# Kernel tuning notes

Hardware: AMD Instinct MI355X
Metric: run time of the kernel (lower is better)

## Reference

```python
import jax, jax.numpy as jnp
import numpy as np

N_DRUG = 572
EMB = 512
K_NB = 64
SEG_NB = 16
BN_EPS = 1e-5


def setup_inputs() -> dict:
    key = jax.random.key(0)
    ks = jax.random.split(key, 8)
    return {
        "drug_name": jnp.arange(N_DRUG, dtype=jnp.int64) if jax.config.jax_enable_x64 else jnp.arange(N_DRUG, dtype=jnp.int32),
        "adj_tail": jax.random.randint(ks[0], (N_DRUG, K_NB), 0, 100000),
        "adj_relation": jax.random.randint(ks[1], (N_DRUG, K_NB), 0, 200),
        "inv_adj_idx": jax.random.randint(ks[2], (N_DRUG, SEG_NB), 0, N_DRUG),
        "drug_table": jax.random.normal(ks[3], (N_DRUG, EMB), dtype=jnp.float32),
        "rela_table": jax.random.normal(ks[4], (200, EMB), dtype=jnp.float32),
        "ent_table": jax.random.normal(ks[5], (100000, EMB), dtype=jnp.float32),
        "W_lin": jax.random.normal(ks[6], (2 * EMB, EMB), dtype=jnp.float32) * (1.0 / np.sqrt(2 * EMB)),
        "b_lin": jnp.zeros((EMB,), jnp.float32),
        "bn_gamma": jnp.ones((EMB,), jnp.float32),
        "bn_beta": jnp.zeros((EMB,), jnp.float32),
        "epoch": 2,
    }


def _forward(drug_name, adj_tail, adj_relation, inv_adj_idx,
             drug_table, rela_table, ent_table, W_lin, b_lin,
             bn_gamma, bn_beta, epoch):
    # Embedding gathers
    drug_emb = drug_table[drug_name]          # [N, D]
    rel_emb = rela_table[adj_relation]        # [N, K, D]
    ent_emb = ent_table[adj_tail]             # [N, K, D]

    # KGCN-style attention over sampled neighbors: score_k = softmax(drug . rel_k)
    scores = jax.nn.softmax(jnp.einsum('nd,nkd->nk', drug_emb, rel_emb), axis=1)
    attended = jnp.einsum('nk,nkd->nd', scores, ent_emb)  # [N, D]

    # Linear -> ReLU -> BatchNorm1d (training-mode batch stats, biased var)
    e = jnp.concatenate([attended, drug_emb], axis=1)     # [N, 2D]
    h = jax.nn.relu(e @ W_lin + b_lin)                    # [N, D]
    mu = jnp.mean(h, axis=0)
    var = jnp.mean(jnp.square(h - mu), axis=0)
    drug_f = bn_gamma * (h - mu) * jax.lax.rsqrt(var + BN_EPS) + bn_beta

    if epoch > 1:
        # Sequential in-place neighbor averaging (faithful to the Python loop:
        # later drugs see already-updated rows).
        def body(f, x):
            i, pos = x
            avg = jnp.mean(f[pos], axis=0)                # [D]
            f = f.at[i].set((avg + f[i]) * 0.5)
            return f, None
        idxs = jnp.arange(N_DRUG)
        drug_f, _ = jax.lax.scan(body, drug_f, (idxs, inv_adj_idx))
    return drug_f


def reference(drug_name, adj_tail, adj_relation, inv_adj_idx,
              drug_table, rela_table, ent_table, W_lin, b_lin,
              bn_gamma, bn_beta, epoch):
    return _forward(drug_name, adj_tail, adj_relation, inv_adj_idx,
                    drug_table, rela_table, ent_table, W_lin, b_lin,
                    bn_gamma, bn_beta, epoch)
```

## Files before the change

kernel.cpp:

```cpp
#include <hip/hip_runtime.h>
#include <hip/hip_bf16.h>

#define N_DRUG 572
#define EMB    512
#define K_NB   64
#define SEG_NB 16
#define SCOLS  16
#define DPB    4

typedef __hip_bfloat16  bf16;
typedef __hip_bfloat162 bf162;

__device__ __forceinline__ float b2f(bf16 x){ return __bfloat162float(x); }

template<typename T> __device__ __forceinline__ float ldf(const T* p);
template<> __device__ __forceinline__ float ldf<float>(const float* p){ return *p; }
template<> __device__ __forceinline__ float ldf<bf16>(const bf16* p){ return b2f(*p); }

template<typename T> __device__ __forceinline__ float2 ld2(const T* p);
template<> __device__ __forceinline__ float2 ld2<float>(const float* p){ return *(const float2*)p; }
template<> __device__ __forceinline__ float2 ld2<bf16>(const bf16* p){
    bf162 v = *(const bf162*)p; return make_float2(b2f(v.x), b2f(v.y));
}

template<typename T> __device__ __forceinline__ void st2(T* p, float x, float y);
template<> __device__ __forceinline__ void st2<float>(float* p, float x, float y){ *(float2*)p = make_float2(x, y); }
template<> __device__ __forceinline__ void st2<bf16>(bf16* p, float x, float y){
    bf162 v; v.x = __float2bfloat16(x); v.y = __float2bfloat16(y); *(bf162*)p = v;
}

__device__ __forceinline__ bool idx_is64(const void* drug_name) {
    return ((const int*)drug_name)[1] == 0;
}
__device__ __forceinline__ int ld_idx(const void* p, int i, bool is64) {
    return is64 ? (int)((const long long*)p)[i] : ((const int*)p)[i];
}

__device__ __forceinline__ bool detect_bf16(const void* tab) {
    const int lane = threadIdx.x & 63;
    int hit = 0;
    if (lane < 32) {
        const unsigned u = ((const unsigned*)tab)[lane * 997];
        const unsigned e = (u >> 7) & 0xffu;
        hit = (e >= 110u && e <= 141u) ? 1 : 0;
    }
    return __popcll(__ballot(hit)) >= 24;
}

struct __align__(16) FwdSmem {
    float e[DPB][2 * EMB];
    float sc[DPB][K_NB];
    int   tl[DPB][K_NB];
    int   rl[DPB][K_NB];
};

template<typename T>
__device__ void fwd_impl(FwdSmem& sm,
    const void* drug_name, const void* adj_tail, const void* adj_rel,
    const T* __restrict__ drug_table, const T* __restrict__ rela_table,
    const T* __restrict__ ent_table,  const T* __restrict__ W,
    const T* __restrict__ bl, T* __restrict__ h)
{
    const int  t    = threadIdx.x;
    const int  n0   = blockIdx.x * DPB;
    const bool is64 = idx_is64(drug_name);

    #pragma unroll
    for (int dr = 0; dr < DPB; ++dr) {
        const int row = ld_idx(drug_name, n0 + dr, is64);
        const float2 v = ld2(drug_table + (size_t)row * EMB + 2 * t);
        sm.e[dr][EMB + 2 * t]     = v.x;
        sm.e[dr][EMB + 2 * t + 1] = v.y;
    }
    {
        const int dr = t >> 6, k = t & 63;
        sm.tl[dr][k] = ld_idx(adj_tail, n0 * K_NB + t, is64);
        sm.rl[dr][k] = ld_idx(adj_rel,  n0 * K_NB + t, is64);
    }
    __syncthreads();

    {
        const int wave = t >> 6, lane = t & 63;
        const int g = lane >> 4, c = lane & 15;
        const float* ed = &sm.e[wave][EMB];
        #pragma unroll 2
        for (int pass = 0; pass < 16; ++pass) {
            const int k = pass * 4 + g;
            const T* rl = rela_table + (size_t)sm.rl[wave][k] * EMB;
            float p = 0.f;
            #pragma unroll
            for (int m = 0; m < 16; ++m) {
                const int dd = 2 * c + 32 * m;
                const float2 rv = ld2(rl + dd);
                const float2 ev = *(const float2*)&ed[dd];
                p = fmaf(ev.x, rv.x, p);
                p = fmaf(ev.y, rv.y, p);
            }
            p += __shfl_xor(p, 1, 64);
            p += __shfl_xor(p, 2, 64);
            p += __shfl_xor(p, 4, 64);
            p += __shfl_xor(p, 8, 64);
            if (c == 0) sm.sc[wave][k] = p;
        }
    }
    __syncthreads();

    {
        const int dr = t >> 6, k = t & 63;
        const float s = sm.sc[dr][k];
        float m = s;
        #pragma unroll
        for (int off = 32; off; off >>= 1) m = fmaxf(m, __shfl_xor(m, off, 64));
        const float ex = __expf(s - m);
        float sum = ex;
        #pragma unroll
        for (int off = 32; off; off >>= 1) sum += __shfl_xor(sum, off, 64);
        sm.sc[dr][k] = ex / sum;
    }
    __syncthreads();

    {
        float a0[DPB], a1[DPB];
        #pragma unroll
        for (int dr = 0; dr < DPB; ++dr) { a0[dr] = 0.f; a1[dr] = 0.f; }
        #pragma unroll 2
        for (int k = 0; k < K_NB; ++k) {
            #pragma unroll
            for (int dr = 0; dr < DPB; ++dr) {
                const float w  = sm.sc[dr][k];
                const float2 v = ld2(ent_table + (size_t)sm.tl[dr][k] * EMB + 2 * t);
                a0[dr] = fmaf(w, v.x, a0[dr]);
                a1[dr] = fmaf(w, v.y, a1[dr]);
            }
        }
        #pragma unroll
        for (int dr = 0; dr < DPB; ++dr) {
            sm.e[dr][2 * t]     = a0[dr];
            sm.e[dr][2 * t + 1] = a1[dr];
        }
    }
    __syncthreads();

    {
        const int d0 = 2 * t;
        const float2 bb = ld2(bl + d0);
        float a0[DPB], a1[DPB];
        #pragma unroll
        for (int dr = 0; dr < DPB; ++dr) { a0[dr] = bb.x; a1[dr] = bb.y; }
        #pragma unroll 2
        for (int q = 0; q < (2 * EMB) / 4; ++q) {
            const T* Wp = W + (size_t)(4 * q) * EMB + d0;
            const float2 w0 = ld2(Wp);
            const float2 w1 = ld2(Wp + EMB);
            const float2 w2 = ld2(Wp + 2 * EMB);
            const float2 w3 = ld2(Wp + 3 * EMB);
            #pragma unroll
            for (int dr = 0; dr < DPB; ++dr) {
                const float4 f = ((const float4*)&sm.e[dr][0])[q];
                a0[dr] = fmaf(f.x, w0.x, a0[dr]); a1[dr] = fmaf(f.x, w0.y, a1[dr]);
                a0[dr] = fmaf(f.y, w1.x, a0[dr]); a1[dr] = fmaf(f.y, w1.y, a1[dr]);
                a0[dr] = fmaf(f.z, w2.x, a0[dr]); a1[dr] = fmaf(f.z, w2.y, a1[dr]);
                a0[dr] = fmaf(f.w, w3.x, a0[dr]); a1[dr] = fmaf(f.w, w3.y, a1[dr]);
            }
        }
        #pragma unroll
        for (int dr = 0; dr < DPB; ++dr)
            st2(h + (size_t)(n0 + dr) * EMB + d0,
                fmaxf(a0[dr], 0.f), fmaxf(a1[dr], 0.f));
    }
}

__global__ __launch_bounds__(256) void k_fwd(
    const void* drug_name, const void* adj_tail, const void* adj_rel,
    const void* drug_tab, const void* rela_tab, const void* ent_tab,
    const void* W, const void* bl, void* h)
{
    __shared__ FwdSmem sm;
    if (detect_bf16(drug_tab))
        fwd_impl<bf16>(sm, drug_name, adj_tail, adj_rel,
                       (const bf16*)drug_tab, (const bf16*)rela_tab,
                       (const bf16*)ent_tab, (const bf16*)W,
                       (const bf16*)bl, (bf16*)h);
    else
        fwd_impl<float>(sm, drug_name, adj_tail, adj_rel,
                        (const float*)drug_tab, (const float*)rela_tab,
                        (const float*)ent_tab, (const float*)W,
                        (const float*)bl, (float*)h);
}

struct __align__(16) ScanSmem {
    float    fbuf[N_DRUG * SCOLS];
    unsigned obuf[N_DRUG * SEG_NB];
    float4   corr[576];
};

__device__ __forceinline__ float bflo(unsigned u){ return __uint_as_float(u << 16); }
__device__ __forceinline__ float bfhi(unsigned u){ return __uint_as_float(u & 0xffff0000u); }
__device__ __forceinline__ unsigned pack_bf2(float a, float b) {
    bf162 v; v.x = __float2bfloat16(a); v.y = __float2bfloat16(b);
    unsigned u; __builtin_memcpy(&u, &v, 4); return u;
}

template<typename T>
__device__ __forceinline__ void stage_fbuf(float* fbuf, const T* h, int c0, int t);
template<>
__device__ __forceinline__ void stage_fbuf<float>(float* fbuf, const float* h, int c0, int t) {
    float4* dst = (float4*)fbuf;
    #pragma unroll 4
    for (int k = t; k < N_DRUG * 4; k += 64)
        dst[k] = *(const float4*)(h + (size_t)(k >> 2) * EMB + c0 + 4 * (k & 3));
}
template<>
__device__ __forceinline__ void stage_fbuf<bf16>(float* fbuf, const bf16* h, int c0, int t) {
    float4* dst = (float4*)fbuf;
    #pragma unroll 4
    for (int k = t; k < N_DRUG * 2; k += 64) {
        const uint4 v = *(const uint4*)(h + (size_t)(k >> 1) * EMB + c0 + 8 * (k & 1));
        dst[2 * k]     = make_float4(bflo(v.x), bfhi(v.x), bflo(v.y), bfhi(v.y));
        dst[2 * k + 1] = make_float4(bflo(v.z), bfhi(v.z), bflo(v.w), bfhi(v.w));
    }
}

template<typename T>
__device__ __forceinline__ void flush_fbuf(const float* fbuf, T* h, int c0, int t);
template<>
__device__ __forceinline__ void flush_fbuf<float>(const float* fbuf, float* h, int c0, int t) {
    const float4* src = (const float4*)fbuf;
    #pragma unroll 4
    for (int k = t; k < N_DRUG * 4; k += 64)
        *(float4*)(h + (size_t)(k >> 2) * EMB + c0 + 4 * (k & 3)) = src[k];
}
template<>
__device__ __forceinline__ void flush_fbuf<bf16>(const float* fbuf, bf16* h, int c0, int t) {
    const float4* src = (const float4*)fbuf;
    #pragma unroll 4
    for (int k = t; k < N_DRUG * 2; k += 64) {
        const float4 f0 = src[2 * k], f1 = src[2 * k + 1];
        uint4 o;
        o.x = pack_bf2(f0.x, f0.y); o.y = pack_bf2(f0.z, f0.w);
        o.z = pack_bf2(f1.x, f1.y); o.w = pack_bf2(f1.z, f1.w);
        *(uint4*)(h + (size_t)(k >> 1) * EMB + c0 + 8 * (k & 1)) = o;
    }
}

template<bool IS64>
__device__ __forceinline__ void stage_obuf(unsigned* obuf, const void* inv, int t) {
    const uint4* src = (const uint4*)inv;
    if (IS64) {
        #pragma unroll 4
        for (int k = t; k < (N_DRUG * SEG_NB) / 2; k += 64) {
            const uint4 v = src[k];
            *(uint2*)(obuf + 2 * k) = make_uint2(v.x << 4, v.z << 4);
        }
    } else {
        uint4* dst = (uint4*)obuf;
        #pragma unroll 4
        for (int k = t; k < (N_DRUG * SEG_NB) / 4; k += 64) {
            uint4 v = src[k];
            v.x <<= 4; v.y <<= 4; v.z <<= 4; v.w <<= 4;
            dst[k] = v;
        }
    }
}

#define RMIN(X) (((X) < N_DRUG) ? (X) : (N_DRUG - 1))

#define BODY4(Vg, Qg, Sc, Fc, Cc, Vr, Sr, I)                                 \
    {                                                                        \
        Vg.x = fb[Qg.x + c]; Vg.y = fb[Qg.y + c];                            \
        Vg.z = fb[Qg.z + c]; Vg.w = fb[Qg.w + c];                            \
        Qg = ob4[RMIN((I) + 7) * 4 + g];                                     \
        float nv = fmaf(Sc, 1.f / 32.f, Fc * 0.5f);                          \
        nv = fmaf(Cc.x, nv1 - f1, nv);                                       \
        nv = fmaf(Cc.y, nv2 - f2, nv);                                       \
        nv = fmaf(Cc.z, nv3 - f3, nv);                                       \
        f3 = f2; f2 = f1; f1 = Fc; nv3 = nv2; nv2 = nv1; nv1 = nv;           \
        if (g == 0) sm.fbuf[(I) * SCOLS + c] = nv;                           \
        Fc = fb[RMIN((I) + 4) * 16 + c];                                     \
        Cc = sm.corr[(I) + 4];                                               \
        float l = (Vr.x + Vr.y) + (Vr.z + Vr.w);                             \
        Sr = (l + __shfl_xor(l, 16, 64)) +                                   \
             (__shfl_xor(l, 32, 64) + __shfl_xor(l, 48, 64));                \
    }

template<typename T, bool IS64>
__device__ void scan_impl(ScanSmem& sm, T* __restrict__ h,
    const void* __restrict__ inv, const T* __restrict__ gamma,
    const T* __restrict__ beta, const void* __restrict__ epoch)
{
    const int t  = threadIdx.x;
    const int c0 = blockIdx.x * SCOLS;

    stage_obuf<IS64>(sm.obuf, inv, t);
    stage_fbuf<T>(sm.fbuf, h, c0, t);
    for (int k = t; k < 576; k += 64) sm.corr[k] = make_float4(0.f, 0.f, 0.f, 0.f);
    __syncthreads();

    for (int i = 1 + t; i < N_DRUG; i += 64) {
        const unsigned tA = (unsigned)(i - 1) << 4;
        const unsigned tB = (unsigned)(i - 2) << 4;
        const unsigned tC = (unsigned)(i - 3) << 4;
        int cA = 0, cB = 0, cC = 0;
        #pragma unroll
        for (int j = 0; j < SEG_NB; ++j) {
            const unsigned o = sm.obuf[i * SEG_NB + j];
            cA += (o == tA) ? 1 : 0;
            cB += (o == tB) ? 1 : 0;
            cC += (o == tC) ? 1 : 0;
        }
        sm.corr[i] = make_float4((float)cA * (1.f / 32.f),
                                 (float)cB * (1.f / 32.f),
                                 (float)cC * (1.f / 32.f), 0.f);
    }

    {
        const int c = t & 15, g = t >> 4;
        float s = 0.f, s2 = 0.f;
        for (int r = g; r < N_DRUG; r += 4) {
            const float x = sm.fbuf[r * SCOLS + c];
            s += x; s2 = fmaf(x, x, s2);
        }
        s  += __shfl_xor(s, 16, 64);  s  += __shfl_xor(s, 32, 64);
        s2 += __shfl_xor(s2, 16, 64); s2 += __shfl_xor(s2, 32, 64);
        const float mu  = s * (1.f / N_DRUG);
        const float var = fmaxf(s2 * (1.f / N_DRUG) - mu * mu, 0.f);
        const float gs  = ldf(gamma + c0 + c) * rsqrtf(var + 1e-5f);
        const float bs  = ldf(beta  + c0 + c);
        for (int r = g; r < N_DRUG; r += 4) {
            const float x = sm.fbuf[r * SCOLS + c];
            sm.fbuf[r * SCOLS + c] = fmaf(x - mu, gs, bs);
        }
    }
    __syncthreads();

    if (((const int*)epoch)[0] > 1) {
        const int c = t & 15, g = t >> 4;
        const float* fb  = sm.fbuf;
        const uint4* ob4 = (const uint4*)sm.obuf;

        float4 V0, V1, V2, V3;
        uint4  Q0, Q1, Q2, Q3;

        {
            const uint4 o0 = ob4[0 * 4 + g], o1 = ob4[1 * 4 + g], o2 = ob4[2 * 4 + g];
            V0.x = fb[o0.x + c]; V0.y = fb[o0.y + c];
            V0.z = fb[o0.z + c]; V0.w = fb[o0.w + c];
            V1.x = fb[o1.x + c]; V1.y = fb[o1.y + c];
            V1.z = fb[o1.z + c]; V1.w = fb[o1.w + c];
            V2.x = fb[o2.x + c]; V2.y = fb[o2.y + c];
            V2.z = fb[o2.z + c]; V2.w = fb[o2.w + c];
        }
        Q3 = ob4[3 * 4 + g];
        Q0 = ob4[4 * 4 + g]; Q1 = ob4[5 * 4 + g]; Q2 = ob4[6 * 4 + g];
        float F0 = fb[0 * 16 + c], F1 = fb[1 * 16 + c];
        float F2 = fb[2 * 16 + c], F3 = fb[3 * 16 + c];
        float4 C0 = sm.corr[0], C1 = sm.corr[1];
        float4 C2 = sm.corr[2], C3 = sm.corr[3];
        float S0, S1, S2 = 0.f, S3 = 0.f;
        {
            float l0 = (V0.x + V0.y) + (V0.z + V0.w);
            S0 = (l0 + __shfl_xor(l0, 16, 64)) +
                 (__shfl_xor(l0, 32, 64) + __shfl_xor(l0, 48, 64));
            float l1 = (V1.x + V1.y) + (V1.z + V1.w);
            S1 = (l1 + __shfl_xor(l1, 16, 64)) +
                 (__shfl_xor(l1, 32, 64) + __shfl_xor(l1, 48, 64));
        }
        float nv1 = 0.f, nv2 = 0.f, nv3 = 0.f, f1 = 0.f, f2 = 0.f, f3 = 0.f;

        for (int i = 0; i < N_DRUG; i += 4) {
            BODY4(V3, Q3, S0, F0, C0, V2, S2, i);
            BODY4(V0, Q0, S1, F1, C1, V3, S3, i + 1);
            BODY4(V1, Q1, S2, F2, C2, V0, S0, i + 2);
            BODY4(V2, Q2, S3, F3, C3, V1, S1, i + 3);
        }
    }
    __syncthreads();

    flush_fbuf<T>(sm.fbuf, h, c0, t);
}

__global__ __launch_bounds__(64) void k_scan(
    void* h, const void* inv, const void* gamma, const void* beta,
    const void* epoch, const void* drug_name, const void* drug_tab)
{
    __shared__ ScanSmem sm;
    const bool isbf = detect_bf16(drug_tab);
    const bool is64 = idx_is64(drug_name);
    if (isbf) {
        if (is64) scan_impl<bf16, true >(sm, (bf16*)h, inv, (const bf16*)gamma, (const bf16*)beta, epoch);
        else      scan_impl<bf16, false>(sm, (bf16*)h, inv, (const bf16*)gamma, (const bf16*)beta, epoch);
    } else {
        if (is64) scan_impl<float, true >(sm, (float*)h, inv, (const float*)gamma, (const float*)beta, epoch);
        else      scan_impl<float, false>(sm, (float*)h, inv, (const float*)gamma, (const float*)beta, epoch);
    }
}

extern "C" void kernel_launch(void* const* d_in, const int* in_sizes, int n_in,
                              void* d_out, int out_size, void* d_ws, size_t ws_size,
                              hipStream_t stream)
{
    (void)in_sizes; (void)n_in; (void)out_size; (void)d_ws; (void)ws_size;

    k_fwd<<<N_DRUG / DPB, 256, 0, stream>>>(
        d_in[0], d_in[1], d_in[2],
        d_in[4], d_in[5], d_in[6],
        d_in[7], d_in[8],
        d_out);
    k_scan<<<EMB / SCOLS, 64, 0, stream>>>(
        d_out, d_in[3],
        d_in[9], d_in[10], d_in[11],
        d_in[0], d_in[4]);
}
```

Before: 442.1 us.

## Process one drug per block with split-K waves and wide vector loads

The forward kernel now handles one drug per block instead of four, launching 572 blocks rather than 143 so more of the GPU's compute units are busy. Each wave takes a quarter of the neighbours, and later a quarter of the GEMV reduction dimension, using 8-element vector loads per lane. Partial sums are combined through shared memory. The cost is that every block rereads the full weight matrix with no reuse across drugs, and extra barriers are added.

```diff
diff --git a/kernel.cpp b/kernel.cpp
--- a/kernel.cpp
+++ b/kernel.cpp
@@ -6,12 +6,17 @@
 #define K_NB   64
 #define SEG_NB 16
 #define SCOLS  16
-#define DPB    4
 
 typedef __hip_bfloat16  bf16;
 typedef __hip_bfloat162 bf162;
 
 __device__ __forceinline__ float b2f(bf16 x){ return __bfloat162float(x); }
+__device__ __forceinline__ float bflo(unsigned u){ return __uint_as_float(u << 16); }
+__device__ __forceinline__ float bfhi(unsigned u){ return __uint_as_float(u & 0xffff0000u); }
+__device__ __forceinline__ unsigned pack_bf2(float a, float b) {
+    bf162 v; v.x = __float2bfloat16(a); v.y = __float2bfloat16(b);
+    unsigned u; __builtin_memcpy(&u, &v, 4); return u;
+}
 
 template<typename T> __device__ __forceinline__ float ldf(const T* p);
 template<> __device__ __forceinline__ float ldf<float>(const float* p){ return *p; }
@@ -27,6 +32,20 @@
 template<> __device__ __forceinline__ void st2<float>(float* p, float x, float y){ *(float2*)p = make_float2(x, y); }
 template<> __device__ __forceinline__ void st2<bf16>(bf16* p, float x, float y){
     bf162 v; v.x = __float2bfloat16(x); v.y = __float2bfloat16(y); *(bf162*)p = v;
+}
+
+struct F8 { float v[8]; };
+template<typename T> __device__ __forceinline__ F8 ld8(const T* p);
+template<> __device__ __forceinline__ F8 ld8<float>(const float* p){
+    F8 r; const float4 a = ((const float4*)p)[0], b = ((const float4*)p)[1];
+    r.v[0]=a.x; r.v[1]=a.y; r.v[2]=a.z; r.v[3]=a.w;
+    r.v[4]=b.x; r.v[5]=b.y; r.v[6]=b.z; r.v[7]=b.w; return r;
+}
+template<> __device__ __forceinline__ F8 ld8<bf16>(const bf16* p){
+    F8 r; const uint4 u = *(const uint4*)p;
+    r.v[0]=bflo(u.x); r.v[1]=bfhi(u.x); r.v[2]=bflo(u.y); r.v[3]=bfhi(u.y);
+    r.v[4]=bflo(u.z); r.v[5]=bfhi(u.z); r.v[6]=bflo(u.w); r.v[7]=bfhi(u.w);
+    return r;
 }
 
 __device__ __forceinline__ bool idx_is64(const void* drug_name) {
@@ -48,10 +67,11 @@
 }
 
 struct __align__(16) FwdSmem {
-    float e[DPB][2 * EMB];
-    float sc[DPB][K_NB];
-    int   tl[DPB][K_NB];
-    int   rl[DPB][K_NB];
+    float e[2 * EMB];
+    float part[4][EMB];
+    float sc[K_NB];
+    int   tl[K_NB];
+    int   rl[K_NB];
 };
 
 template<typename T>
@@ -62,52 +82,47 @@
     const T* __restrict__ bl, T* __restrict__ h)
 {
     const int  t    = threadIdx.x;
-    const int  n0   = blockIdx.x * DPB;
+    const int  wave = t >> 6, lane = t & 63;
+    const int  n    = blockIdx.x;
     const bool is64 = idx_is64(drug_name);
 
-    #pragma unroll
-    for (int dr = 0; dr < DPB; ++dr) {
-        const int row = ld_idx(drug_name, n0 + dr, is64);
+    {
+        const int row = ld_idx(drug_name, n, is64);
         const float2 v = ld2(drug_table + (size_t)row * EMB + 2 * t);
-        sm.e[dr][EMB + 2 * t]     = v.x;
-        sm.e[dr][EMB + 2 * t + 1] = v.y;
-    }
-    {
-        const int dr = t >> 6, k = t & 63;
-        sm.tl[dr][k] = ld_idx(adj_tail, n0 * K_NB + t, is64);
-        sm.rl[dr][k] = ld_idx(adj_rel,  n0 * K_NB + t, is64);
-    }
-    __syncthreads();
-
-    {
-        const int wave = t >> 6, lane = t & 63;
-        const int g = lane >> 4, c = lane & 15;
-        const float* ed = &sm.e[wave][EMB];
-        #pragma unroll 2
-        for (int pass = 0; pass < 16; ++pass) {
-            const int k = pass * 4 + g;
-            const T* rl = rela_table + (size_t)sm.rl[wave][k] * EMB;
+        sm.e[EMB + 2 * t]     = v.x;
+        sm.e[EMB + 2 * t + 1] = v.y;
+        if (t < K_NB) {
+            sm.tl[t] = ld_idx(adj_tail, n * K_NB + t, is64);
+            sm.rl[t] = ld_idx(adj_rel,  n * K_NB + t, is64);
+        }
+    }
+    __syncthreads();
+
+    F8 ed;
+    {
+        const float4 e0 = ((const float4*)&sm.e[EMB + 8 * lane])[0];
+        const float4 e1 = ((const float4*)&sm.e[EMB + 8 * lane])[1];
+        ed.v[0]=e0.x; ed.v[1]=e0.y; ed.v[2]=e0.z; ed.v[3]=e0.w;
+        ed.v[4]=e1.x; ed.v[5]=e1.y; ed.v[6]=e1.z; ed.v[7]=e1.w;
+    }
+
+    {
+        #pragma unroll 4
+        for (int kk = 0; kk < 16; ++kk) {
+            const int k = 16 * wave + kk;
+            const F8 rv = ld8(rela_table + (size_t)sm.rl[k] * EMB + 8 * lane);
             float p = 0.f;
             #pragma unroll
-            for (int m = 0; m < 16; ++m) {
-                const int dd = 2 * c + 32 * m;
-                const float2 rv = ld2(rl + dd);
-                const float2 ev = *(const float2*)&ed[dd];
-                p = fmaf(ev.x, rv.x, p);
-                p = fmaf(ev.y, rv.y, p);
-            }
-            p += __shfl_xor(p, 1, 64);
-            p += __shfl_xor(p, 2, 64);
-            p += __shfl_xor(p, 4, 64);
-            p += __shfl_xor(p, 8, 64);
-            if (c == 0) sm.sc[wave][k] = p;
-        }
-    }
-    __syncthreads();
-
-    {
-        const int dr = t >> 6, k = t & 63;
-        const float s = sm.sc[dr][k];
+            for (int m = 0; m < 8; ++m) p = fmaf(ed.v[m], rv.v[m], p);
+            #pragma unroll
+            for (int off = 32; off; off >>= 1) p += __shfl_xor(p, off, 64);
+            if (lane == 0) sm.sc[k] = p;
+        }
+    }
+    __syncthreads();
+
+    if (t < 64) {
+        const float s = sm.sc[t];
         float m = s;
         #pragma unroll
         for (int off = 32; off; off >>= 1) m = fmaxf(m, __shfl_xor(m, off, 64));
@@ -115,58 +130,68 @@
         float sum = ex;
         #pragma unroll
         for (int off = 32; off; off >>= 1) sum += __shfl_xor(sum, off, 64);
-        sm.sc[dr][k] = ex / sum;
-    }
-    __syncthreads();
-
-    {
-        float a0[DPB], a1[DPB];
-        #pragma unroll
-        for (int dr = 0; dr < DPB; ++dr) { a0[dr] = 0.f; a1[dr] = 0.f; }
-        #pragma unroll 2
-        for (int k = 0; k < K_NB; ++k) {
+        sm.sc[t] = ex / sum;
+    }
+    __syncthreads();
+
+    {
+        float a[8];
+        #pragma unroll
+        for (int m = 0; m < 8; ++m) a[m] = 0.f;
+        #pragma unroll 4
+        for (int kk = 0; kk < 16; ++kk) {
+            const int k = 16 * wave + kk;
+            const float wgt = sm.sc[k];
+            const F8 v = ld8(ent_table + (size_t)sm.tl[k] * EMB + 8 * lane);
             #pragma unroll
-            for (int dr = 0; dr < DPB; ++dr) {
-                const float w  = sm.sc[dr][k];
-                const float2 v = ld2(ent_table + (size_t)sm.tl[dr][k] * EMB + 2 * t);
-                a0[dr] = fmaf(w, v.x, a0[dr]);
-                a1[dr] = fmaf(w, v.y, a1[dr]);
-            }
-        }
-        #pragma unroll
-        for (int dr = 0; dr < DPB; ++dr) {
-            sm.e[dr][2 * t]     = a0[dr];
-            sm.e[dr][2 * t + 1] = a1[dr];
-        }
+            for (int m = 0; m < 8; ++m) a[m] = fmaf(wgt, v.v[m], a[m]);
+        }
+        float4* pp = (float4*)&sm.part[wave][8 * lane];
+        pp[0] = make_float4(a[0], a[1], a[2], a[3]);
+        pp[1] = make_float4(a[4], a[5], a[6], a[7]);
+    }
+    __syncthreads();
+
+    {
+        float2 s = make_float2(0.f, 0.f);
+        #pragma unroll
+        for (int w = 0; w < 4; ++w) {
+            const float2 pw = *(const float2*)&sm.part[w][2 * t];
+            s.x += pw.x; s.y += pw.y;
+        }
+        sm.e[2 * t]     = s.x;
+        sm.e[2 * t + 1] = s.y;
+    }
+    __syncthreads();
+
+    {
+        float acc[8];
+        #pragma unroll
+        for (int m = 0; m < 8; ++m) acc[m] = 0.f;
+        const int j0 = wave * 256;
+        #pragma unroll 4
+        for (int j = 0; j < 256; ++j) {
+            const float ej = sm.e[j0 + j];
+            const F8 w8 = ld8(W + (size_t)(j0 + j) * EMB + 8 * lane);
+            #pragma unroll
+            for (int m = 0; m < 8; ++m) acc[m] = fmaf(ej, w8.v[m], acc[m]);
+        }
+        float4* pp = (float4*)&sm.part[wave][8 * lane];
+        pp[0] = make_float4(acc[0], acc[1], acc[2], acc[3]);
+        pp[1] = make_float4(acc[4], acc[5], acc[6], acc[7]);
     }
     __syncthreads();
 
     {
         const int d0 = 2 * t;
         const float2 bb = ld2(bl + d0);
-        float a0[DPB], a1[DPB];
-        #pragma unroll
-        for (int dr = 0; dr < DPB; ++dr) { a0[dr] = bb.x; a1[dr] = bb.y; }
-        #pragma unroll 2
-        for (int q = 0; q < (2 * EMB) / 4; ++q) {
-            const T* Wp = W + (size_t)(4 * q) * EMB + d0;
-            const float2 w0 = ld2(Wp);
-            const float2 w1 = ld2(Wp + EMB);
-            const float2 w2 = ld2(Wp + 2 * EMB);
-            const float2 w3 = ld2(Wp + 3 * EMB);
-            #pragma unroll
-            for (int dr = 0; dr < DPB; ++dr) {
-                const float4 f = ((const float4*)&sm.e[dr][0])[q];
-                a0[dr] = fmaf(f.x, w0.x, a0[dr]); a1[dr] = fmaf(f.x, w0.y, a1[dr]);
-                a0[dr] = fmaf(f.y, w1.x, a0[dr]); a1[dr] = fmaf(f.y, w1.y, a1[dr]);
-                a0[dr] = fmaf(f.z, w2.x, a0[dr]); a1[dr] = fmaf(f.z, w2.y, a1[dr]);
-                a0[dr] = fmaf(f.w, w3.x, a0[dr]); a1[dr] = fmaf(f.w, w3.y, a1[dr]);
-            }
-        }
-        #pragma unroll
-        for (int dr = 0; dr < DPB; ++dr)
-            st2(h + (size_t)(n0 + dr) * EMB + d0,
-                fmaxf(a0[dr], 0.f), fmaxf(a1[dr], 0.f));
+        float x = bb.x, y = bb.y;
+        #pragma unroll
+        for (int w = 0; w < 4; ++w) {
+            const float2 pw = *(const float2*)&sm.part[w][d0];
+            x += pw.x; y += pw.y;
+        }
+        st2(h + (size_t)n * EMB + d0, fmaxf(x, 0.f), fmaxf(y, 0.f));
     }
 }
 
@@ -194,13 +219,6 @@
     float4   corr[576];
 };
 
-__device__ __forceinline__ float bflo(unsigned u){ return __uint_as_float(u << 16); }
-__device__ __forceinline__ float bfhi(unsigned u){ return __uint_as_float(u & 0xffff0000u); }
-__device__ __forceinline__ unsigned pack_bf2(float a, float b) {
-    bf162 v; v.x = __float2bfloat16(a); v.y = __float2bfloat16(b);
-    unsigned u; __builtin_memcpy(&u, &v, 4); return u;
-}
-
 template<typename T>
 __device__ __forceinline__ void stage_fbuf(float* fbuf, const T* h, int c0, int t);
 template<>
@@ -401,7 +419,7 @@
 {
     (void)in_sizes; (void)n_in; (void)out_size; (void)d_ws; (void)ws_size;
 
-    k_fwd<<<N_DRUG / DPB, 256, 0, stream>>>(
+    k_fwd<<<N_DRUG, 256, 0, stream>>>(
         d_in[0], d_in[1], d_in[2],
         d_in[4], d_in[5], d_in[6],
         d_in[7], d_in[8],
```

New measurement: 418.0 us. 5.5% less time.
